# Optimization experiments

Measured on AMD Instinct MI355X. Metric: run time of the kernel, lower is better.

Reference implementation:

```python
import jax, jax.numpy as jnp
import numpy as np

B, C, H, W = 512, 3, 64, 32
K = 2                      # fractional pool kernel size
HOUT, WOUT = 38, 16        # floor(64*0.6), floor(32*0.5)
HID = 128                  # RNN hidden size
D = C * HOUT               # RNN input size = 114


def _frac_starts(in_size, out_size, k, u=0.5):
    # PyTorch fractional-max-pool interval formula with deterministic sample u
    alpha = (in_size - k) / (out_size - 1)
    i = np.arange(out_size - 1)
    starts = np.floor((i + u) * alpha) - np.floor(u * alpha)
    return np.concatenate([starts, [in_size - k]]).astype(np.int32)

ROW = _frac_starts(H, HOUT, K)   # (HOUT,) window start rows
COL = _frac_starts(W, WOUT, K)   # (WOUT,) window start cols


def setup_inputs() -> dict:
    key = jax.random.key(0)
    ks = jax.random.split(key, 5)
    s = 1.0 / np.sqrt(HID)  # torch RNNCell init scale
    return {
        "x": jax.random.normal(ks[0], (B, C, H, W), jnp.float32),
        "W_ih": jax.random.uniform(ks[1], (HID, D), jnp.float32, -s, s),
        "W_hh": jax.random.uniform(ks[2], (HID, HID), jnp.float32, -s, s),
        "b_ih": jax.random.uniform(ks[3], (HID,), jnp.float32, -s, s),
        "b_hh": jax.random.uniform(ks[4], (HID,), jnp.float32, -s, s),
    }


def reference(x, W_ih, W_hh, b_ih, b_hh):
    # 1) fractional max pool, kernel 2: pairwise max over gathered window starts
    xr = jnp.maximum(x[:, :, ROW, :], x[:, :, ROW + 1, :])          # (B,C,HOUT,W)
    pooled = jnp.maximum(xr[:, :, :, COL], xr[:, :, :, COL + 1])    # (B,C,HOUT,WOUT)
    # 2) exact (erf-based) GELU, matching torch nn.GELU default
    act = jax.nn.gelu(pooled, approximate=False)
    # 3) sequence over width: (WOUT, B, C*HOUT), C-major flatten matches torch view
    seq = act.transpose(3, 0, 1, 2).reshape(WOUT, B, D)
    # 4) vanilla RNNCell across time via scan
    def step(h, xt):
        h = jnp.tanh(xt @ W_ih.T + b_ih + h @ W_hh.T + b_hh)
        return h, h
    _, outs = jax.lax.scan(step, jnp.zeros((B, HID), x.dtype), seq)  # (WOUT,B,HID)
    # 5) temporal mean + tanh
    t_mean = jnp.tanh(outs.mean(axis=0))                             # (B,HID)
    # 6) modulate by global spatial mean of pooled; torch broadcasting of
    #    (B,HID) * (B,1,1,1) yields (B,1,B,HID) — replicated faithfully
    s_mean = pooled.mean(axis=(1, 2, 3), keepdims=True)              # (B,1,1,1)
    return t_mean * s_mean                                           # (B,1,B,HID)
```

## Files before the change

kernel.cpp:

```cpp
#include <hip/hip_runtime.h>
#include <math.h>

#define BB   512
#define CC   3
#define HH   64
#define WW   32
#define HOUT 38
#define WOUT 16
#define HID  128
#define DD   114
#define SEQP 120
#define WIHP 120
#define WHHP 132
#define NPOOL (CC*HOUT*WOUT)
#define XPAIR (2*CC*HH*WW)

typedef float f32x4 __attribute__((ext_vector_type(4)));

__device__ __forceinline__ float fast_tanh(float u) {
    return 1.f - 2.f / (__expf(2.f * u) + 1.f);
}

#define WS_SMEAN 0
#define WS_TMEAN 512

__global__ __launch_bounds__(256, 1)
void k1_fused(const float* __restrict__ x,
              const float* __restrict__ Wih,
              const float* __restrict__ Whh,
              const float* __restrict__ bih,
              const float* __restrict__ bhh,
              float* __restrict__ s_mean,
              float* __restrict__ t_mean)
{
    __shared__ __align__(16) float wst[HID * WHHP];
    __shared__ __align__(16) float seq0[WOUT][SEQP];
    __shared__ __align__(16) float seq1[WOUT][SEQP];
    __shared__ __align__(16) float hb0[2][HID];
    __shared__ __align__(16) float hb1[2][HID];
    __shared__ float red[2][4];
    __shared__ int   rowl[HOUT];

    const int tid  = threadIdx.x;
    const int wid  = tid >> 6;
    const int lane = tid & 63;
    const int kl   = (wid << 5) | (lane & 31);
    const int kc   = lane >> 5;
    const int b0   = 2 * blockIdx.x;

    f32x4 xpf[12];
    {
        const f32x4* xg = (const f32x4*)(x + (size_t)b0 * (CC*HH*WW));
        #pragma unroll
        for (int i = 0; i < 12; ++i) xpf[i] = xg[tid + 256*i];
    }
    f32x4 wihpf[14], wihtail;
    {
        const f32x4* wg = (const f32x4*)Wih;
        #pragma unroll
        for (int i = 0; i < 14; ++i) wihpf[i] = wg[tid + 256*i];
        if (tid < 64) wihtail = wg[3584 + tid];
    }

    if (tid < HOUT) {
        double alpha = (double)(HH - 2) / (double)(HOUT - 1);
        rowl[tid] = (tid < HOUT - 1)
            ? (int)(floor((tid + 0.5) * alpha) - floor(0.5 * alpha))
            : (HH - 2);
    }
    if (tid < HID) { hb0[0][tid] = 0.f; hb1[0][tid] = 0.f; }
    if (tid < 96) {
        seq0[tid / 6][DD + tid % 6] = 0.f;
        seq1[tid / 6][DD + tid % 6] = 0.f;
    }

    {
        f32x4* xd = (f32x4*)wst;
        #pragma unroll
        for (int i = 0; i < 12; ++i) xd[tid + 256*i] = xpf[i];
    }
    __syncthreads();

    float ps0 = 0.f, ps1 = 0.f;
    #pragma unroll
    for (int it = 0; it < 15; ++it) {
        int idx = tid + it*256;
        if (idx < 2*NPOOL) {
            int bsel = (idx >= NPOOL);
            int r0   = idx - bsel*NPOOL;
            int c  = r0 / (HOUT*WOUT);
            int r  = r0 % (HOUT*WOUT);
            int ho = r / WOUT;
            int wo = r % WOUT;
            const float* p0 = &wst[bsel*(CC*HH*WW) + c*(HH*WW) + rowl[ho]*WW + 2*wo];
            float m = fmaxf(fmaxf(p0[0], p0[1]), fmaxf(p0[WW], p0[WW+1]));
            float a = 0.5f * m * (1.f + erff(m * 0.70710678118654752440f));
            if (bsel) { ps1 += m; seq1[wo][c*HOUT + ho] = a; }
            else      { ps0 += m; seq0[wo][c*HOUT + ho] = a; }
        }
    }
    #pragma unroll
    for (int off = 32; off > 0; off >>= 1) {
        ps0 += __shfl_down(ps0, off);
        ps1 += __shfl_down(ps1, off);
    }
    if (lane == 0) { red[0][wid] = ps0; red[1][wid] = ps1; }
    __syncthreads();
    if (tid < 2)
        s_mean[b0 + tid] = (red[tid][0] + red[tid][1] + red[tid][2] + red[tid][3])
                           * (1.f / (float)NPOOL);

    #pragma unroll
    for (int i = 0; i < 14; ++i) {
        int j = 4*(tid + 256*i);
        #pragma unroll
        for (int e = 0; e < 4; ++e) {
            int r  = (j + e) / DD;
            int cc = (j + e) - r*DD;
            wst[r*WIHP + cc] = wihpf[i][e];
        }
    }
    if (tid < 64) {
        int j = 4*(3584 + tid);
        #pragma unroll
        for (int e = 0; e < 4; ++e) {
            int r  = (j + e) / DD;
            int cc = (j + e) - r*DD;
            wst[r*WIHP + cc] = wihtail[e];
        }
    }
    for (int j = tid; j < HID*6; j += 256)
        wst[(j/6)*WIHP + DD + (j % 6)] = 0.f;
    __syncthreads();

    f32x4 wih[15];
    {
        const f32x4* wr = (const f32x4*)&wst[kl*WIHP + kc*60];
        #pragma unroll
        for (int dd = 0; dd < 15; ++dd) wih[dd] = wr[dd];
    }

    f32x4 whhpf[16];
    {
        const f32x4* hg = (const f32x4*)Whh;
        #pragma unroll
        for (int i = 0; i < 16; ++i) whhpf[i] = hg[tid + 256*i];
    }

    float zr0[WOUT], zr1[WOUT];
    #pragma unroll
    for (int t = 0; t < WOUT; ++t) {
        const f32x4* a4 = (const f32x4*)&seq0[t][kc*60];
        const f32x4* c4 = (const f32x4*)&seq1[t][kc*60];
        float s0 = 0.f, s1 = 0.f, s2 = 0.f, s3 = 0.f;
        float u0 = 0.f, u1 = 0.f, u2 = 0.f, u3 = 0.f;
        #pragma unroll
        for (int dd = 0; dd < 15; ++dd) {
            f32x4 a = a4[dd], c = c4[dd], w = wih[dd];
            s0 = fmaf(w.x, a.x, s0); u0 = fmaf(w.x, c.x, u0);
            s1 = fmaf(w.y, a.y, s1); u1 = fmaf(w.y, c.y, u1);
            s2 = fmaf(w.z, a.z, s2); u2 = fmaf(w.z, c.z, u2);
            s3 = fmaf(w.w, a.w, s3); u3 = fmaf(w.w, c.w, u3);
        }
        float p = (s0 + s1) + (s2 + s3);
        float q = (u0 + u1) + (u2 + u3);
        zr0[t] = p + __shfl_xor(p, 32);
        zr1[t] = q + __shfl_xor(q, 32);
    }
    {
        const float bias = bih[kl] + bhh[kl];
        #pragma unroll
        for (int t = 0; t < WOUT; ++t) { zr0[t] += bias; zr1[t] += bias; }
    }
    __syncthreads();

    #pragma unroll
    for (int i = 0; i < 16; ++i) {
        int j4 = tid + 256*i;
        *(f32x4*)&wst[(j4 >> 5)*WHHP + ((j4 & 31) << 2)] = whhpf[i];
    }
    __syncthreads();
    f32x4 whh[16];
    {
        const f32x4* wr = (const f32x4*)&wst[kl*WHHP + (kc << 6)];
        #pragma unroll
        for (int dd = 0; dd < 16; ++dd) whh[dd] = wr[dd];
    }

    float hsum0 = 0.f, hsum1 = 0.f;
    #pragma unroll
    for (int t = 0; t < WOUT; ++t) {
        const int cur = t & 1, nxt = cur ^ 1;
        const f32x4* h40 = (const f32x4*)&hb0[cur][kc << 6];
        const f32x4* h41 = (const f32x4*)&hb1[cur][kc << 6];
        float s0 = 0.f, s1 = 0.f, s2 = 0.f, s3 = 0.f;
        float u0 = 0.f, u1 = 0.f, u2 = 0.f, u3 = 0.f;
        #pragma unroll
        for (int dd = 0; dd < 16; ++dd) {
            f32x4 hv = h40[dd], gv = h41[dd], w = whh[dd];
            s0 = fmaf(w.x, hv.x, s0); u0 = fmaf(w.x, gv.x, u0);
            s1 = fmaf(w.y, hv.y, s1); u1 = fmaf(w.y, gv.y, u1);
            s2 = fmaf(w.z, hv.z, s2); u2 = fmaf(w.z, gv.z, u2);
            s3 = fmaf(w.w, hv.w, s3); u3 = fmaf(w.w, gv.w, u3);
        }
        float p  = (s0 + s1) + (s2 + s3);
        float q  = (u0 + u1) + (u2 + u3);
        float v0 = zr0[t] + p + __shfl_xor(p, 32);
        float v1 = zr1[t] + q + __shfl_xor(q, 32);
        float hn0 = fast_tanh(v0);
        float hn1 = fast_tanh(v1);
        hsum0 += hn0; hsum1 += hn1;
        if (kc == 0) { hb0[nxt][kl] = hn0; hb1[nxt][kl] = hn1; }
        __syncthreads();
    }
    if (kc == 0) {
        t_mean[(b0    )*HID + kl] = fast_tanh(hsum0 * (1.f / 16.f));
        t_mean[(b0 + 1)*HID + kl] = fast_tanh(hsum1 * (1.f / 16.f));
    }
}

__global__ __launch_bounds__(256)
void k2_out(const float* __restrict__ s_mean,
            const float* __restrict__ t_mean,
            f32x4* __restrict__ out)
{
    const int i   = blockIdx.x >> 3;
    const int sub = blockIdx.x & 7;
    const float s = s_mean[i];
    const f32x4* t4 = (const f32x4*)t_mean + sub*2048;
    f32x4*       o  = out + (size_t)i*16384 + sub*2048;
    const int tid = threadIdx.x;
    #pragma unroll
    for (int j = 0; j < 8; ++j) {
        int idx = tid + j*256;
        o[idx] = s * t4[idx];
    }
}

extern "C" void kernel_launch(void* const* d_in, const int* in_sizes, int n_in,
                              void* d_out, int out_size, void* d_ws, size_t ws_size,
                              hipStream_t stream)
{
    const float* x   = (const float*)d_in[0];
    const float* Wih = (const float*)d_in[1];
    const float* Whh = (const float*)d_in[2];
    const float* bih = (const float*)d_in[3];
    const float* bhh = (const float*)d_in[4];

    float* ws     = (float*)d_ws;
    float* s_mean = ws + WS_SMEAN;
    float* t_mean = ws + WS_TMEAN;

    k1_fused<<<dim3(BB/2), dim3(256), 0, stream>>>(x, Wih, Whh, bih, bhh, s_mean, t_mean);
    k2_out  <<<dim3(4096), dim3(256), 0, stream>>>(s_mean, t_mean, (f32x4*)d_out);
}
```

Before: 55.10 us.

## Fuse output broadcast into main kernel via grid barrier and widen blocks to 512 threads

Merges the two kernels into one. Each block finishes its RNN work, then waits at a global atomic-counter barrier and writes its two slices of the (B,1,B,HID) output, so s_mean stays in shared memory and the second launch disappears. Blocks grow to 512 threads, which splits each hidden unit's dot products across four lanes instead of two and needs one more shuffle stage. The sequence and hidden buffers are padded to 36-float chunks to cut LDS bank conflicts. This relies on all 256 blocks being resident at the same time, adds a memset launch, and uses a bounded spin loop that could give wrong output if co-residency fails.

After: 133.5 us. 2.42x slower.

```diff
diff --git a/kernel.cpp b/kernel.cpp
--- a/kernel.cpp
+++ b/kernel.cpp
@@ -2,6 +2,7 @@
 #include <math.h>
 
 #define BB   512
+#define NBLK 256
 #define CC   3
 #define HH   64
 #define WW   32
@@ -9,11 +10,11 @@
 #define WOUT 16
 #define HID  128
 #define DD   114
-#define SEQP 120
-#define WIHP 120
+#define SEQQ 36
+#define SEQP 144
+#define WIHP 132
 #define WHHP 132
 #define NPOOL (CC*HOUT*WOUT)
-#define XPAIR (2*CC*HH*WW)
 
 typedef float f32x4 __attribute__((ext_vector_type(4)));
 
@@ -21,44 +22,45 @@
     return 1.f - 2.f / (__expf(2.f * u) + 1.f);
 }
 
-#define WS_SMEAN 0
-#define WS_TMEAN 512
-
-__global__ __launch_bounds__(256, 1)
-void k1_fused(const float* __restrict__ x,
-              const float* __restrict__ Wih,
-              const float* __restrict__ Whh,
-              const float* __restrict__ bih,
-              const float* __restrict__ bhh,
-              float* __restrict__ s_mean,
-              float* __restrict__ t_mean)
+#define WS_CNT_OFF 262144
+
+__global__ __launch_bounds__(512, 2)
+void k_fused(const float* __restrict__ x,
+             const float* __restrict__ Wih,
+             const float* __restrict__ Whh,
+             const float* __restrict__ bih,
+             const float* __restrict__ bhh,
+             float* __restrict__ t_mean,
+             int*   __restrict__ bar_cnt,
+             f32x4* __restrict__ out)
 {
     __shared__ __align__(16) float wst[HID * WHHP];
     __shared__ __align__(16) float seq0[WOUT][SEQP];
     __shared__ __align__(16) float seq1[WOUT][SEQP];
-    __shared__ __align__(16) float hb0[2][HID];
-    __shared__ __align__(16) float hb1[2][HID];
-    __shared__ float red[2][4];
+    __shared__ __align__(16) float hb0[2][SEQP];
+    __shared__ __align__(16) float hb1[2][SEQP];
+    __shared__ float red[2][8];
+    __shared__ float sm[2];
     __shared__ int   rowl[HOUT];
 
     const int tid  = threadIdx.x;
     const int wid  = tid >> 6;
     const int lane = tid & 63;
-    const int kl   = (wid << 5) | (lane & 31);
-    const int kc   = lane >> 5;
+    const int kl   = (wid << 4) | (lane & 15);
+    const int kc   = lane >> 4;
     const int b0   = 2 * blockIdx.x;
 
-    f32x4 xpf[12];
+    f32x4 xpf[6];
     {
         const f32x4* xg = (const f32x4*)(x + (size_t)b0 * (CC*HH*WW));
         #pragma unroll
-        for (int i = 0; i < 12; ++i) xpf[i] = xg[tid + 256*i];
-    }
-    f32x4 wihpf[14], wihtail;
+        for (int i = 0; i < 6; ++i) xpf[i] = xg[tid + 512*i];
+    }
+    f32x4 wihpf[7], wihtail;
     {
         const f32x4* wg = (const f32x4*)Wih;
         #pragma unroll
-        for (int i = 0; i < 14; ++i) wihpf[i] = wg[tid + 256*i];
+        for (int i = 0; i < 7; ++i) wihpf[i] = wg[tid + 512*i];
         if (tid < 64) wihtail = wg[3584 + tid];
     }
 
@@ -68,23 +70,28 @@
             ? (int)(floor((tid + 0.5) * alpha) - floor(0.5 * alpha))
             : (HH - 2);
     }
-    if (tid < HID) { hb0[0][tid] = 0.f; hb1[0][tid] = 0.f; }
-    if (tid < 96) {
-        seq0[tid / 6][DD + tid % 6] = 0.f;
-        seq1[tid / 6][DD + tid % 6] = 0.f;
+    if (tid < HID) {
+        hb0[0][SEQQ*(tid >> 5) + (tid & 31)] = 0.f;
+        hb1[0][SEQQ*(tid >> 5) + (tid & 31)] = 0.f;
+    }
+    if (tid < 448) {
+        int s  = tid >= 224;
+        int r0 = tid - s*224;
+        int t = r0 / 14, o = 18 + r0 % 14;
+        if (s) seq1[t][3*SEQQ + o] = 0.f; else seq0[t][3*SEQQ + o] = 0.f;
     }
 
     {
         f32x4* xd = (f32x4*)wst;
         #pragma unroll
-        for (int i = 0; i < 12; ++i) xd[tid + 256*i] = xpf[i];
+        for (int i = 0; i < 6; ++i) xd[tid + 512*i] = xpf[i];
     }
     __syncthreads();
 
     float ps0 = 0.f, ps1 = 0.f;
     #pragma unroll
-    for (int it = 0; it < 15; ++it) {
-        int idx = tid + it*256;
+    for (int it = 0; it < 8; ++it) {
+        int idx = tid + it*512;
         if (idx < 2*NPOOL) {
             int bsel = (idx >= NPOOL);
             int r0   = idx - bsel*NPOOL;
@@ -95,8 +102,10 @@
             const float* p0 = &wst[bsel*(CC*HH*WW) + c*(HH*WW) + rowl[ho]*WW + 2*wo];
             float m = fmaxf(fmaxf(p0[0], p0[1]), fmaxf(p0[WW], p0[WW+1]));
             float a = 0.5f * m * (1.f + erff(m * 0.70710678118654752440f));
-            if (bsel) { ps1 += m; seq1[wo][c*HOUT + ho] = a; }
-            else      { ps0 += m; seq0[wo][c*HOUT + ho] = a; }
+            int d = c*HOUT + ho;
+            int off = SEQQ*(d >> 5) + (d & 31);
+            if (bsel) { ps1 += m; seq1[wo][off] = a; }
+            else      { ps0 += m; seq0[wo][off] = a; }
         }
     }
     #pragma unroll
@@ -106,13 +115,16 @@
     }
     if (lane == 0) { red[0][wid] = ps0; red[1][wid] = ps1; }
     __syncthreads();
-    if (tid < 2)
-        s_mean[b0 + tid] = (red[tid][0] + red[tid][1] + red[tid][2] + red[tid][3])
-                           * (1.f / (float)NPOOL);
-
-    #pragma unroll
-    for (int i = 0; i < 14; ++i) {
-        int j = 4*(tid + 256*i);
+    if (tid < 2) {
+        float r = 0.f;
+        #pragma unroll
+        for (int i = 0; i < 8; ++i) r += red[tid][i];
+        sm[tid] = r * (1.f / (float)NPOOL);
+    }
+
+    #pragma unroll
+    for (int i = 0; i < 7; ++i) {
+        int j = 4*(tid + 512*i);
         #pragma unroll
         for (int e = 0; e < 4; ++e) {
             int r  = (j + e) / DD;
@@ -129,33 +141,33 @@
             wst[r*WIHP + cc] = wihtail[e];
         }
     }
-    for (int j = tid; j < HID*6; j += 256)
-        wst[(j/6)*WIHP + DD + (j % 6)] = 0.f;
-    __syncthreads();
-
-    f32x4 wih[15];
-    {
-        const f32x4* wr = (const f32x4*)&wst[kl*WIHP + kc*60];
-        #pragma unroll
-        for (int dd = 0; dd < 15; ++dd) wih[dd] = wr[dd];
-    }
-
-    f32x4 whhpf[16];
+    for (int j = tid; j < HID*14; j += 512)
+        wst[(j/14)*WIHP + DD + (j % 14)] = 0.f;
+    __syncthreads();
+
+    f32x4 wih[8];
+    {
+        const f32x4* wr = (const f32x4*)&wst[kl*WIHP + (kc << 5)];
+        #pragma unroll
+        for (int dd = 0; dd < 8; ++dd) wih[dd] = wr[dd];
+    }
+
+    f32x4 whhpf[8];
     {
         const f32x4* hg = (const f32x4*)Whh;
         #pragma unroll
-        for (int i = 0; i < 16; ++i) whhpf[i] = hg[tid + 256*i];
+        for (int i = 0; i < 8; ++i) whhpf[i] = hg[tid + 512*i];
     }
 
     float zr0[WOUT], zr1[WOUT];
     #pragma unroll
     for (int t = 0; t < WOUT; ++t) {
-        const f32x4* a4 = (const f32x4*)&seq0[t][kc*60];
-        const f32x4* c4 = (const f32x4*)&seq1[t][kc*60];
-        float s0 = 0.f, s1 = 0.f, s2 = 0.f, s3 = 0.f;
-        float u0 = 0.f, u1 = 0.f, u2 = 0.f, u3 = 0.f;
-        #pragma unroll
-        for (int dd = 0; dd < 15; ++dd) {
+        const f32x4* a4 = (const f32x4*)&seq0[t][kc*SEQQ];
+        const f32x4* c4 = (const f32x4*)&seq1[t][kc*SEQQ];
+        float s0=0.f, s1=0.f, s2=0.f, s3=0.f;
+        float u0=0.f, u1=0.f, u2=0.f, u3=0.f;
+        #pragma unroll
+        for (int dd = 0; dd < 8; ++dd) {
             f32x4 a = a4[dd], c = c4[dd], w = wih[dd];
             s0 = fmaf(w.x, a.x, s0); u0 = fmaf(w.x, c.x, u0);
             s1 = fmaf(w.y, a.y, s1); u1 = fmaf(w.y, c.y, u1);
@@ -164,6 +176,8 @@
         }
         float p = (s0 + s1) + (s2 + s3);
         float q = (u0 + u1) + (u2 + u3);
+        p += __shfl_xor(p, 16);
+        q += __shfl_xor(q, 16);
         zr0[t] = p + __shfl_xor(p, 32);
         zr1[t] = q + __shfl_xor(q, 32);
     }
@@ -175,65 +189,81 @@
     __syncthreads();
 
     #pragma unroll
-    for (int i = 0; i < 16; ++i) {
-        int j4 = tid + 256*i;
+    for (int i = 0; i < 8; ++i) {
+        int j4 = tid + 512*i;
         *(f32x4*)&wst[(j4 >> 5)*WHHP + ((j4 & 31) << 2)] = whhpf[i];
     }
     __syncthreads();
-    f32x4 whh[16];
-    {
-        const f32x4* wr = (const f32x4*)&wst[kl*WHHP + (kc << 6)];
-        #pragma unroll
-        for (int dd = 0; dd < 16; ++dd) whh[dd] = wr[dd];
+    f32x4 whh[8];
+    {
+        const f32x4* wr = (const f32x4*)&wst[kl*WHHP + (kc << 5)];
+        #pragma unroll
+        for (int dd = 0; dd < 8; ++dd) whh[dd] = wr[dd];
     }
 
     float hsum0 = 0.f, hsum1 = 0.f;
     #pragma unroll
     for (int t = 0; t < WOUT; ++t) {
         const int cur = t & 1, nxt = cur ^ 1;
-        const f32x4* h40 = (const f32x4*)&hb0[cur][kc << 6];
-        const f32x4* h41 = (const f32x4*)&hb1[cur][kc << 6];
-        float s0 = 0.f, s1 = 0.f, s2 = 0.f, s3 = 0.f;
-        float u0 = 0.f, u1 = 0.f, u2 = 0.f, u3 = 0.f;
-        #pragma unroll
-        for (int dd = 0; dd < 16; ++dd) {
+        const f32x4* h40 = (const f32x4*)&hb0[cur][kc*SEQQ];
+        const f32x4* h41 = (const f32x4*)&hb1[cur][kc*SEQQ];
+        float s0=0.f, s1=0.f, s2=0.f, s3=0.f;
+        float u0=0.f, u1=0.f, u2=0.f, u3=0.f;
+        #pragma unroll
+        for (int dd = 0; dd < 8; ++dd) {
             f32x4 hv = h40[dd], gv = h41[dd], w = whh[dd];
             s0 = fmaf(w.x, hv.x, s0); u0 = fmaf(w.x, gv.x, u0);
             s1 = fmaf(w.y, hv.y, s1); u1 = fmaf(w.y, gv.y, u1);
             s2 = fmaf(w.z, hv.z, s2); u2 = fmaf(w.z, gv.z, u2);
             s3 = fmaf(w.w, hv.w, s3); u3 = fmaf(w.w, gv.w, u3);
         }
-        float p  = (s0 + s1) + (s2 + s3);
-        float q  = (u0 + u1) + (u2 + u3);
+        float p = (s0 + s1) + (s2 + s3);
+        float q = (u0 + u1) + (u2 + u3);
+        p += __shfl_xor(p, 16);
+        q += __shfl_xor(q, 16);
         float v0 = zr0[t] + p + __shfl_xor(p, 32);
         float v1 = zr1[t] + q + __shfl_xor(q, 32);
         float hn0 = fast_tanh(v0);
         float hn1 = fast_tanh(v1);
         hsum0 += hn0; hsum1 += hn1;
-        if (kc == 0) { hb0[nxt][kl] = hn0; hb1[nxt][kl] = hn1; }
+        if (kc == 0) {
+            int off = SEQQ*(kl >> 5) + (kl & 31);
+            hb0[nxt][off] = hn0;
+            hb1[nxt][off] = hn1;
+        }
         __syncthreads();
     }
     if (kc == 0) {
         t_mean[(b0    )*HID + kl] = fast_tanh(hsum0 * (1.f / 16.f));
         t_mean[(b0 + 1)*HID + kl] = fast_tanh(hsum1 * (1.f / 16.f));
     }
-}
-
-__global__ __launch_bounds__(256)
-void k2_out(const float* __restrict__ s_mean,
-            const float* __restrict__ t_mean,
-            f32x4* __restrict__ out)
-{
-    const int i   = blockIdx.x >> 3;
-    const int sub = blockIdx.x & 7;
-    const float s = s_mean[i];
-    const f32x4* t4 = (const f32x4*)t_mean + sub*2048;
-    f32x4*       o  = out + (size_t)i*16384 + sub*2048;
-    const int tid = threadIdx.x;
-    #pragma unroll
-    for (int j = 0; j < 8; ++j) {
-        int idx = tid + j*256;
-        o[idx] = s * t4[idx];
+
+    __threadfence();
+    __syncthreads();
+    if (tid == 0) {
+        __hip_atomic_fetch_add(bar_cnt, 1, __ATOMIC_ACQ_REL, __HIP_MEMORY_SCOPE_AGENT);
+        int iters = 0;
+        while (__hip_atomic_load(bar_cnt, __ATOMIC_ACQUIRE, __HIP_MEMORY_SCOPE_AGENT) < NBLK
+               && iters < 2000000) {
+            __builtin_amdgcn_s_sleep(8);
+            ++iters;
+        }
+    }
+    __syncthreads();
+    __threadfence();
+
+    {
+        const float  s0 = sm[0], s1 = sm[1];
+        const f32x4* t4 = (const f32x4*)t_mean;
+        f32x4* o0 = out + (size_t)b0 * 16384;
+        f32x4* o1 = o0 + 16384;
+        #pragma unroll
+        for (int j = 0; j < 32; ++j) {
+            int idx = tid + 512*j;
+            f32x4 v = t4[idx];
+            o0[idx] = s0 * v;
+            o1[idx] = s1 * v;
+        }
     }
 }
 
@@ -247,10 +277,10 @@
     const float* bih = (const float*)d_in[3];
     const float* bhh = (const float*)d_in[4];
 
-    float* ws     = (float*)d_ws;
-    float* s_mean = ws + WS_SMEAN;
-    float* t_mean = ws + WS_TMEAN;
-
-    k1_fused<<<dim3(BB/2), dim3(256), 0, stream>>>(x, Wih, Whh, bih, bhh, s_mean, t_mean);
-    k2_out  <<<dim3(4096), dim3(256), 0, stream>>>(s_mean, t_mean, (f32x4*)d_out);
+    float* t_mean  = (float*)d_ws;
+    int*   bar_cnt = (int*)((char*)d_ws + WS_CNT_OFF);
+
+    hipMemsetAsync(bar_cnt, 0, sizeof(int), stream);
+    k_fused<<<dim3(NBLK), dim3(512), 0, stream>>>(
+        x, Wih, Whh, bih, bhh, t_mean, bar_cnt, (f32x4*)d_out);
 }
```
